# Optimization experiments

Measured on AMD Instinct MI355X. Metric: run time of the kernel, lower is better.

## Reference

```python
import jax, jax.numpy as jnp
import numpy as np

TAU = 0.07
MARGIN = 0.2
NUM_SPECIES = 64  # matches fill_max of species_ids


def _l2norm(x):
    return x / jnp.linalg.norm(x, axis=-1, keepdims=True)


def setup_inputs() -> dict:
    key = jax.random.key(0)
    k1, k2, k3 = jax.random.split(key, 3)
    B, D = 8192, 256
    species_embed = _l2norm(jax.random.normal(k1, (B, D), dtype=jnp.float32))
    text_embed = _l2norm(jax.random.normal(k2, (B, D), dtype=jnp.float32))
    species_ids = jax.random.randint(k3, (B,), 0, NUM_SPECIES, dtype=jnp.int32)
    return {"species_embed": species_embed, "text_embed": text_embed,
            "species_ids": species_ids}


def reference(species_embed, text_embed, species_ids):
    B = species_embed.shape[0]
    dtype = species_embed.dtype

    sim = species_embed @ text_embed.T                      # (B, B)
    same = species_ids[:, None] == species_ids[None, :]     # (B, B) bool, symmetric
    diag_sim = jnp.diagonal(sim)                            # (B,)

    # ---- intra-species symmetric InfoNCE (per-species CE, averaged over species)
    logits = sim / TAU
    neg_inf = jnp.finfo(dtype).min
    masked = jnp.where(same, logits, neg_inf)               # restrict to same-species cols
    diag_logit = diag_sim / TAU
    ce_v2t = jax.scipy.special.logsumexp(masked, axis=1) - diag_logit   # per-row CE
    ce_t2v = jax.scipy.special.logsumexp(masked.T, axis=1) - diag_logit # transpose: same mask is symmetric

    ones = jnp.ones((B,), dtype=dtype)
    counts = jax.ops.segment_sum(ones, species_ids, num_segments=NUM_SPECIES)          # group sizes
    seg_v2t = jax.ops.segment_sum(ce_v2t, species_ids, num_segments=NUM_SPECIES)
    seg_t2v = jax.ops.segment_sum(ce_t2v, species_ids, num_segments=NUM_SPECIES)
    valid_s = counts >= 2                                   # groups with <2 members skipped
    per_species = (seg_v2t + seg_t2v) / (2.0 * jnp.maximum(counts, 1.0))
    n_valid = jnp.maximum(jnp.sum(valid_s.astype(dtype)), 1.0)
    loss_infonce = jnp.sum(jnp.where(valid_s, per_species, 0.0)) / n_valid

    # ---- cross-species triplet (pos = mean same-species sim excl. self, neg = mean diff-species sim)
    same_f = same.astype(dtype)
    row_same_sum = jnp.sum(sim * same_f, axis=1)            # includes diagonal
    row_sum = jnp.sum(sim, axis=1)
    pos_cnt = jnp.sum(same_f, axis=1) - 1.0
    neg_cnt = B - jnp.sum(same_f, axis=1)
    pos_mean = (row_same_sum - diag_sim) / jnp.maximum(pos_cnt, 1.0)
    neg_mean = (row_sum - row_same_sum) / jnp.maximum(neg_cnt, 1.0)
    tri = jax.nn.relu(neg_mean - pos_mean + MARGIN)
    valid_i = (pos_cnt > 0) & (neg_cnt > 0)
    n_valid_i = jnp.maximum(jnp.sum(valid_i.astype(dtype)), 1.0)
    loss_triplet = jnp.sum(jnp.where(valid_i, tri, 0.0)) / n_valid_i

    return loss_infonce + loss_triplet
```

## Files before the change

### kernel.cpp

```cpp
#include <hip/hip_runtime.h>
#include <hip/hip_fp16.h>

#define TAU 0.07f
#define MARGIN 0.2f
#define NSPEC 64
#define BB 8192
#define DD 256

#define WS_SCALARS   0
#define WS_COUNTS    288
#define WS_OFFSETS   544
#define WS_LSEROW    1024
#define WS_LSECOL    33792
#define WS_TS        66560
#define WS_T         132096
#define WS_ZERO_BYTES 133120
#define WS_DIAG      133632
#define WS_MEMBER    166400
#define WS_TRI       199168

typedef _Float16 half8 __attribute__((ext_vector_type(8)));
typedef float float4v __attribute__((ext_vector_type(4)));
typedef unsigned int uint4v __attribute__((ext_vector_type(4)));

#define NB5 512
#define NB45 (NB5 + BB/4)

__device__ __forceinline__ uint4v pack8(float4 a, float4 b) {
  half8 h;
  h[0] = (_Float16)a.x; h[1] = (_Float16)a.y; h[2] = (_Float16)a.z; h[3] = (_Float16)a.w;
  h[4] = (_Float16)b.x; h[5] = (_Float16)b.y; h[6] = (_Float16)b.z; h[7] = (_Float16)b.w;
  return __builtin_bit_cast(uint4v, h);
}

__global__ void k1_all(const int* __restrict__ ids, char* ws, int* counts_g,
                       int* offsets_g, int* memberList, float* scalars) {
  __shared__ int cnt[NSPEC];
  __shared__ int off[NSPEC];
  int tid = threadIdx.x;
  float4* z = (float4*)ws;
  float4 z4 = make_float4(0.f, 0.f, 0.f, 0.f);
  for (int u = tid; u < WS_ZERO_BYTES / 16; u += 1024) z[u] = z4;
  if (tid < NSPEC) cnt[tid] = 0;
  __syncthreads();
  int myS[8], myP[8];
  #pragma unroll
  for (int r = 0; r < 8; ++r) {
    int i = r * 1024 + tid;
    int s = ids[i];
    myS[r] = s;
    myP[r] = atomicAdd(&cnt[s], 1);
  }
  __syncthreads();
  if (tid < NSPEC) {
    int o = 0;
    for (int t = 0; t < NSPEC; ++t) o += (t < tid) ? cnt[t] : 0;
    off[tid] = o;
    offsets_g[tid] = o;
    int c = cnt[tid];
    counts_g[tid] = c;
    unsigned long long bv = __ballot(c >= 2);
    float nvi = (c >= 2 && c <= BB - 1) ? (float)c : 0.f;
    for (int o2 = 1; o2 < 64; o2 <<= 1) nvi += __shfl_xor(nvi, o2);
    if (tid == 0) {
      scalars[2] = (float)__popcll(bv);
      scalars[3] = nvi;
    }
  }
  __syncthreads();
  #pragma unroll
  for (int r = 0; r < 8; ++r) {
    int i = r * 1024 + tid;
    memberList[off[myS[r]] + myP[r]] = i;
  }
}

__global__ void k2_ts(const float* __restrict__ tx, const int* __restrict__ counts,
                      const int* __restrict__ offsets, const int* __restrict__ memberList,
                      float* Ts) {
  int s = blockIdx.x, r = blockIdx.y;
  int m = counts[s], g0 = offsets[s];
  int k0 = (m * r) >> 3, k1 = (m * (r + 1)) >> 3;
  if (k0 >= k1) return;
  int d = threadIdx.x;
  float acc = 0.f;
  for (int k = k0; k < k1; ++k) acc += tx[memberList[g0 + k] * DD + d];
  atomicAdd(&Ts[s * DD + d], acc);
}

__global__ void k2b_t(const float* __restrict__ Ts, float* T) {
  int d = threadIdx.x;
  float acc = 0.f;
  for (int s = 0; s < NSPEC; ++s) acc += Ts[s * DD + d];
  T[d] = acc;
}

__global__ void k45(const float* __restrict__ sp, const float* __restrict__ tx,
                    const int* __restrict__ ids, const int* __restrict__ counts,
                    const int* __restrict__ offsets, const int* __restrict__ memberList,
                    const float* __restrict__ Ts, const float* __restrict__ T,
                    float* diag, float* tri, float* lseRow, float* lseCol) {
  __shared__ uint4v lds5[1536];
  int tid = threadIdx.x;

  if (blockIdx.x >= NB5) {
    int gt = (blockIdx.x - NB5) * 256 + tid;
    int i = gt >> 6, lane = gt & 63;
    float4 a = *reinterpret_cast<const float4*>(sp + i * DD + lane * 4);
    float4 b = *reinterpret_cast<const float4*>(tx + i * DD + lane * 4);
    float4 tv = *reinterpret_cast<const float4*>(T + lane * 4);
    int s = ids[i];
    int m = counts[s];
    float4 c = *reinterpret_cast<const float4*>(Ts + s * DD + lane * 4);
    float dDiag = a.x * b.x + a.y * b.y + a.z * b.z + a.w * b.w;
    float dT    = a.x * tv.x + a.y * tv.y + a.z * tv.z + a.w * tv.w;
    float dTs   = a.x * c.x + a.y * c.y + a.z * c.z + a.w * c.w;
    #pragma unroll
    for (int o = 1; o < 64; o <<= 1) {
      dDiag += __shfl_xor(dDiag, o);
      dT    += __shfl_xor(dT, o);
      dTs   += __shfl_xor(dTs, o);
    }
    if (lane == 0) {
      diag[i] = dDiag;
      float posMean = (dTs - dDiag) / fmaxf((float)(m - 1), 1.f);
      float negMean = (dT - dTs) / fmaxf((float)(BB - m), 1.f);
      float t = fmaxf(negMean - posMean + MARGIN, 0.f);
      tri[i] = (m >= 2 && m <= BB - 1) ? t : 0.f;
    }
    return;
  }

  int s = blockIdx.x >> 3;
  int sub = blockIdx.x & 7;
  int rt0 = sub >> 1;
  int ct0 = sub & 1;
  int m = counts[s];
  int g0 = offsets[s];
  int lane = tid & 63, wv = tid >> 6;
  int quad = lane >> 4, cl = lane & 15;

  for (int rt = rt0; rt * 64 < m; rt += 4) {
    for (int ct = ct0; ct * 128 < m; ct += 2) {
      float4v acc[8];
      #pragma unroll
      for (int cf = 0; cf < 8; ++cf) acc[cf] = (float4v){0.f, 0.f, 0.f, 0.f};

      for (int kc = 0; kc < 4; ++kc) {
        __syncthreads();
        #pragma unroll
        for (int p = 0; p < 6; ++p) {
          int u = p * 256 + tid;
          int isB = u >= 512;
          int v = isB ? (u - 512) : u;
          int row = v >> 3;
          int subu = v & 7;
          int ksl = subu >> 2, q = subu & 3;
          int d0 = kc * 64 + ksl * 32 + q * 8;
          int idx = isB ? (ct * 128 + row) : (rt * 64 + row);
          uint4v val = (uint4v){0u, 0u, 0u, 0u};
          if (idx < m) {
            const float* src = (isB ? tx : sp) + memberList[g0 + idx] * DD + d0;
            float4 f0 = *reinterpret_cast<const float4*>(src);
            float4 f1 = *reinterpret_cast<const float4*>(src + 4);
            val = pack8(f0, f1);
          }
          int qs = q ^ ((row >> 1) & 3);
          int dst = isB ? (512 + (ksl * 128 + row) * 4 + qs)
                        : ((ksl * 64 + row) * 4 + qs);
          lds5[dst] = val;
        }
        __syncthreads();
        #pragma unroll
        for (int ksl = 0; ksl < 2; ++ksl) {
          int ar = wv * 16 + cl;
          half8 a = __builtin_bit_cast(half8,
              lds5[(ksl * 64 + ar) * 4 + (quad ^ ((ar >> 1) & 3))]);
          #pragma unroll
          for (int cf = 0; cf < 8; ++cf) {
            int br = cf * 16 + cl;
            half8 b = __builtin_bit_cast(half8,
                lds5[512 + (ksl * 128 + br) * 4 + (quad ^ ((br >> 1) & 3))]);
            acc[cf] = __builtin_amdgcn_mfma_f32_16x16x32_f16(a, b, acc[cf], 0, 0, 0);
          }
        }
      }

      int riBase = rt * 64 + wv * 16 + quad * 4;
      float rowAcc[4] = {0.f, 0.f, 0.f, 0.f};
      #pragma unroll
      for (int cf = 0; cf < 8; ++cf) {
        int ci = ct * 128 + cf * 16 + cl;
        bool cv = ci < m;
        float colAcc = 0.f;
        #pragma unroll
        for (int reg = 0; reg < 4; ++reg) {
          bool rv = (riBase + reg) < m;
          float e = (rv && cv) ? __expf(acc[cf][reg] * (1.f / TAU)) : 0.f;
          rowAcc[reg] += e;
          colAcc += e;
        }
        colAcc += __shfl_xor(colAcc, 16);
        colAcc += __shfl_xor(colAcc, 32);
        if (quad == 0 && cv) atomicAdd(&lseCol[g0 + ci], colAcc);
      }
      #pragma unroll
      for (int reg = 0; reg < 4; ++reg) {
        float v = rowAcc[reg];
        v += __shfl_xor(v, 1);
        v += __shfl_xor(v, 2);
        v += __shfl_xor(v, 4);
        v += __shfl_xor(v, 8);
        if (cl == 0 && (riBase + reg) < m) atomicAdd(&lseRow[g0 + riBase + reg], v);
      }
    }
  }
}

__global__ void k67_info(const int* __restrict__ memberList, const int* __restrict__ ids,
                         const int* __restrict__ counts, const float* __restrict__ lseRow,
                         const float* __restrict__ lseCol, const float* __restrict__ diag,
                         const float* __restrict__ tri, float* scalars, float* out) {
  __shared__ float red[8];
  int g = blockIdx.x * blockDim.x + threadIdx.x;
  int i = memberList[g];
  int s = ids[i];
  int m = counts[s];
  float tt = tri[i];
  float term = 0.f;
  if (m >= 2) {
    term = (__logf(lseRow[g]) + __logf(lseCol[g]) - 2.f * diag[i] * (1.f / TAU)) /
           (2.f * (float)m);
  }
  #pragma unroll
  for (int o = 1; o < 64; o <<= 1) {
    term += __shfl_xor(term, o);
    tt += __shfl_xor(tt, o);
  }
  int wv = threadIdx.x >> 6, lane = threadIdx.x & 63;
  if (lane == 0) { red[wv] = term; red[4 + wv] = tt; }
  __syncthreads();
  if (threadIdx.x == 0) {
    atomicAdd(&scalars[1], red[0] + red[1] + red[2] + red[3]);
    atomicAdd(&scalars[0], red[4] + red[5] + red[6] + red[7]);
    __builtin_amdgcn_s_waitcnt(0);
    int old = atomicAdd((int*)&scalars[4], 1);
    if (old == (int)gridDim.x - 1) {
      float info = atomicAdd(&scalars[1], 0.f);
      float trs  = atomicAdd(&scalars[0], 0.f);
      out[0] = info / fmaxf(scalars[2], 1.f) + trs / fmaxf(scalars[3], 1.f);
    }
  }
}

extern "C" void kernel_launch(void* const* d_in, const int* in_sizes, int n_in,
                              void* d_out, int out_size, void* d_ws, size_t ws_size,
                              hipStream_t stream) {
  const float* sp = (const float*)d_in[0];
  const float* tx = (const float*)d_in[1];
  const int* ids = (const int*)d_in[2];
  float* out = (float*)d_out;

  char* ws = (char*)d_ws;
  float* scalars = (float*)(ws + WS_SCALARS);
  int* counts = (int*)(ws + WS_COUNTS);
  int* offsets = (int*)(ws + WS_OFFSETS);
  float* lseRow = (float*)(ws + WS_LSEROW);
  float* lseCol = (float*)(ws + WS_LSECOL);
  float* Ts = (float*)(ws + WS_TS);
  float* T = (float*)(ws + WS_T);
  float* diag = (float*)(ws + WS_DIAG);
  int* memberList = (int*)(ws + WS_MEMBER);
  float* tri = (float*)(ws + WS_TRI);

  k1_all<<<1, 1024, 0, stream>>>(ids, ws, counts, offsets, memberList, scalars);
  k2_ts<<<dim3(NSPEC, 8), 256, 0, stream>>>(tx, counts, offsets, memberList, Ts);
  k2b_t<<<1, 256, 0, stream>>>(Ts, T);
  k45<<<NB45, 256, 0, stream>>>(sp, tx, ids, counts, offsets, memberList, Ts, T,
                                diag, tri, lseRow, lseCol);
  k67_info<<<BB / 256, 256, 0, stream>>>(memberList, ids, counts, lseRow, lseCol,
                                         diag, tri, scalars, out);
}
```

Baseline: 111.3 us.

## Fold same-species sums into LSE tile epilogue and cut launch count

Same-species row sums of sim are now taken from the MFMA tiles already computed for the LSE, instead of a gathered per-species text-sum pass (Ts). The global text column sum T is computed by extra blocks of the first kernel and reduced by one extra block in the LSE kernel. Diagonal and triplet work moves into the final reduction kernel, and its global atomics are spread over 64 buckets. This removes two kernel launches and the gather pass, at the cost of an extra atomic per row in the tile epilogue and fp16-precision positive sums.

```diff
diff --git a/kernel.cpp b/kernel.cpp
--- a/kernel.cpp
+++ b/kernel.cpp
@@ -8,23 +8,24 @@
 #define DD 256
 
 #define WS_SCALARS   0
-#define WS_COUNTS    288
-#define WS_OFFSETS   544
-#define WS_LSEROW    1024
-#define WS_LSECOL    33792
-#define WS_TS        66560
-#define WS_T         132096
-#define WS_ZERO_BYTES 133120
-#define WS_DIAG      133632
-#define WS_MEMBER    166400
-#define WS_TRI       199168
+#define WS_BUCKET    64
+#define WS_COUNTS    8256
+#define WS_OFFSETS   8512
+#define WS_LSEROW    8768
+#define WS_LSECOL    41536
+#define WS_RAWROW    74304
+#define WS_ZERO_BYTES 107072
+#define WS_POSG      107072
+#define WS_MEMBER    139840
+#define WS_TPART     172608
+#define WS_T         303680
 
 typedef _Float16 half8 __attribute__((ext_vector_type(8)));
 typedef float float4v __attribute__((ext_vector_type(4)));
 typedef unsigned int uint4v __attribute__((ext_vector_type(4)));
 
 #define NB5 512
-#define NB45 (NB5 + BB/4)
+#define NTP 128
 
 __device__ __forceinline__ uint4v pack8(float4 a, float4 b) {
   half8 h;
@@ -33,11 +34,27 @@
   return __builtin_bit_cast(uint4v, h);
 }
 
-__global__ void k1_all(const int* __restrict__ ids, char* ws, int* counts_g,
-                       int* offsets_g, int* memberList, float* scalars) {
+__global__ void k1_all(const int* __restrict__ ids, const float* __restrict__ tx,
+                       char* ws, int* counts_g, int* offsets_g,
+                       int* memberList, int* posg, float* Tpart, float* scalars) {
+  int tid = threadIdx.x;
+  if (blockIdx.x > 0) {
+    __shared__ float part[4][256];
+    int b = blockIdx.x - 1;
+    int d = tid & 255;
+    int rq = tid >> 8;
+    int r0 = b * 64 + rq * 16;
+    float acc = 0.f;
+    #pragma unroll 4
+    for (int k = 0; k < 16; ++k) acc += tx[(r0 + k) * DD + d];
+    part[rq][d] = acc;
+    __syncthreads();
+    if (tid < 256)
+      Tpart[b * 256 + tid] = part[0][tid] + part[1][tid] + part[2][tid] + part[3][tid];
+    return;
+  }
   __shared__ int cnt[NSPEC];
   __shared__ int off[NSPEC];
-  int tid = threadIdx.x;
   float4* z = (float4*)ws;
   float4 z4 = make_float4(0.f, 0.f, 0.f, 0.f);
   for (int u = tid; u < WS_ZERO_BYTES / 16; u += 1024) z[u] = z4;
@@ -71,63 +88,24 @@
   #pragma unroll
   for (int r = 0; r < 8; ++r) {
     int i = r * 1024 + tid;
-    memberList[off[myS[r]] + myP[r]] = i;
-  }
-}
-
-__global__ void k2_ts(const float* __restrict__ tx, const int* __restrict__ counts,
-                      const int* __restrict__ offsets, const int* __restrict__ memberList,
-                      float* Ts) {
-  int s = blockIdx.x, r = blockIdx.y;
-  int m = counts[s], g0 = offsets[s];
-  int k0 = (m * r) >> 3, k1 = (m * (r + 1)) >> 3;
-  if (k0 >= k1) return;
-  int d = threadIdx.x;
-  float acc = 0.f;
-  for (int k = k0; k < k1; ++k) acc += tx[memberList[g0 + k] * DD + d];
-  atomicAdd(&Ts[s * DD + d], acc);
-}
-
-__global__ void k2b_t(const float* __restrict__ Ts, float* T) {
-  int d = threadIdx.x;
-  float acc = 0.f;
-  for (int s = 0; s < NSPEC; ++s) acc += Ts[s * DD + d];
-  T[d] = acc;
-}
-
-__global__ void k45(const float* __restrict__ sp, const float* __restrict__ tx,
-                    const int* __restrict__ ids, const int* __restrict__ counts,
-                    const int* __restrict__ offsets, const int* __restrict__ memberList,
-                    const float* __restrict__ Ts, const float* __restrict__ T,
-                    float* diag, float* tri, float* lseRow, float* lseCol) {
+    int g = off[myS[r]] + myP[r];
+    memberList[g] = i;
+    posg[i] = g;
+  }
+}
+
+__global__ void k5_lse(const float* __restrict__ sp, const float* __restrict__ tx,
+                       const int* __restrict__ counts, const int* __restrict__ offsets,
+                       const int* __restrict__ memberList,
+                       const float* __restrict__ Tpart, float* T,
+                       float* lseRow, float* lseCol, float* rawRow) {
   __shared__ uint4v lds5[1536];
   int tid = threadIdx.x;
 
-  if (blockIdx.x >= NB5) {
-    int gt = (blockIdx.x - NB5) * 256 + tid;
-    int i = gt >> 6, lane = gt & 63;
-    float4 a = *reinterpret_cast<const float4*>(sp + i * DD + lane * 4);
-    float4 b = *reinterpret_cast<const float4*>(tx + i * DD + lane * 4);
-    float4 tv = *reinterpret_cast<const float4*>(T + lane * 4);
-    int s = ids[i];
-    int m = counts[s];
-    float4 c = *reinterpret_cast<const float4*>(Ts + s * DD + lane * 4);
-    float dDiag = a.x * b.x + a.y * b.y + a.z * b.z + a.w * b.w;
-    float dT    = a.x * tv.x + a.y * tv.y + a.z * tv.z + a.w * tv.w;
-    float dTs   = a.x * c.x + a.y * c.y + a.z * c.z + a.w * c.w;
-    #pragma unroll
-    for (int o = 1; o < 64; o <<= 1) {
-      dDiag += __shfl_xor(dDiag, o);
-      dT    += __shfl_xor(dT, o);
-      dTs   += __shfl_xor(dTs, o);
-    }
-    if (lane == 0) {
-      diag[i] = dDiag;
-      float posMean = (dTs - dDiag) / fmaxf((float)(m - 1), 1.f);
-      float negMean = (dT - dTs) / fmaxf((float)(BB - m), 1.f);
-      float t = fmaxf(negMean - posMean + MARGIN, 0.f);
-      tri[i] = (m >= 2 && m <= BB - 1) ? t : 0.f;
-    }
+  if (blockIdx.x == NB5) {
+    float acc = 0.f;
+    for (int b = 0; b < NTP; ++b) acc += Tpart[b * 256 + tid];
+    T[tid] = acc;
     return;
   }
 
@@ -188,6 +166,7 @@
 
       int riBase = rt * 64 + wv * 16 + quad * 4;
       float rowAcc[4] = {0.f, 0.f, 0.f, 0.f};
+      float rawAcc[4] = {0.f, 0.f, 0.f, 0.f};
       #pragma unroll
       for (int cf = 0; cf < 8; ++cf) {
         int ci = ct * 128 + cf * 16 + cl;
@@ -196,8 +175,11 @@
         #pragma unroll
         for (int reg = 0; reg < 4; ++reg) {
           bool rv = (riBase + reg) < m;
-          float e = (rv && cv) ? __expf(acc[cf][reg] * (1.f / TAU)) : 0.f;
+          bool on = rv && cv;
+          float sv = on ? acc[cf][reg] : 0.f;
+          float e = on ? __expf(sv * (1.f / TAU)) : 0.f;
           rowAcc[reg] += e;
+          rawAcc[reg] += sv;
           colAcc += e;
         }
         colAcc += __shfl_xor(colAcc, 16);
@@ -207,49 +189,80 @@
       #pragma unroll
       for (int reg = 0; reg < 4; ++reg) {
         float v = rowAcc[reg];
-        v += __shfl_xor(v, 1);
-        v += __shfl_xor(v, 2);
-        v += __shfl_xor(v, 4);
-        v += __shfl_xor(v, 8);
-        if (cl == 0 && (riBase + reg) < m) atomicAdd(&lseRow[g0 + riBase + reg], v);
+        float w = rawAcc[reg];
+        v += __shfl_xor(v, 1);  w += __shfl_xor(w, 1);
+        v += __shfl_xor(v, 2);  w += __shfl_xor(w, 2);
+        v += __shfl_xor(v, 4);  w += __shfl_xor(w, 4);
+        v += __shfl_xor(v, 8);  w += __shfl_xor(w, 8);
+        if (cl == 0 && (riBase + reg) < m) {
+          atomicAdd(&lseRow[g0 + riBase + reg], v);
+          atomicAdd(&rawRow[g0 + riBase + reg], w);
+        }
       }
     }
   }
 }
 
-__global__ void k67_info(const int* __restrict__ memberList, const int* __restrict__ ids,
-                         const int* __restrict__ counts, const float* __restrict__ lseRow,
-                         const float* __restrict__ lseCol, const float* __restrict__ diag,
-                         const float* __restrict__ tri, float* scalars, float* out) {
+__global__ void k67_info(const float* __restrict__ sp, const float* __restrict__ tx,
+                         const int* __restrict__ ids, const int* __restrict__ counts,
+                         const int* __restrict__ posg, const float* __restrict__ T,
+                         const float* __restrict__ lseRow, const float* __restrict__ lseCol,
+                         const float* __restrict__ rawRow, char* ws, float* scalars,
+                         float* out) {
   __shared__ float red[8];
-  int g = blockIdx.x * blockDim.x + threadIdx.x;
-  int i = memberList[g];
-  int s = ids[i];
-  int m = counts[s];
-  float tt = tri[i];
-  float term = 0.f;
-  if (m >= 2) {
-    term = (__logf(lseRow[g]) + __logf(lseCol[g]) - 2.f * diag[i] * (1.f / TAU)) /
-           (2.f * (float)m);
-  }
+  __shared__ int isLast;
+  int tid = threadIdx.x;
+  int wv = tid >> 6, lane = tid & 63;
+  int i = blockIdx.x * 4 + wv;
+
+  float4 a = *reinterpret_cast<const float4*>(sp + i * DD + lane * 4);
+  float4 b = *reinterpret_cast<const float4*>(tx + i * DD + lane * 4);
+  float4 tv = *reinterpret_cast<const float4*>(T + lane * 4);
+  float dDiag = a.x * b.x + a.y * b.y + a.z * b.z + a.w * b.w;
+  float dT    = a.x * tv.x + a.y * tv.y + a.z * tv.z + a.w * tv.w;
   #pragma unroll
   for (int o = 1; o < 64; o <<= 1) {
-    term += __shfl_xor(term, o);
-    tt += __shfl_xor(tt, o);
-  }
-  int wv = threadIdx.x >> 6, lane = threadIdx.x & 63;
-  if (lane == 0) { red[wv] = term; red[4 + wv] = tt; }
-  __syncthreads();
-  if (threadIdx.x == 0) {
-    atomicAdd(&scalars[1], red[0] + red[1] + red[2] + red[3]);
-    atomicAdd(&scalars[0], red[4] + red[5] + red[6] + red[7]);
+    dDiag += __shfl_xor(dDiag, o);
+    dT    += __shfl_xor(dT, o);
+  }
+  if (lane == 0) {
+    int s = ids[i];
+    int m = counts[s];
+    int g = posg[i];
+    float rr = rawRow[g];
+    float info = 0.f;
+    if (m >= 2) {
+      info = (__logf(lseRow[g]) + __logf(lseCol[g]) - 2.f * dDiag * (1.f / TAU)) /
+             (2.f * (float)m);
+    }
+    float posMean = (rr - dDiag) / fmaxf((float)(m - 1), 1.f);
+    float negMean = (dT - rr) / fmaxf((float)(BB - m), 1.f);
+    float t = fmaxf(negMean - posMean + MARGIN, 0.f);
+    float tri = (m >= 2 && m <= BB - 1) ? t : 0.f;
+    red[wv] = info;
+    red[4 + wv] = tri;
+  }
+  __syncthreads();
+  if (tid == 0) {
+    float* bucket = (float*)(ws + WS_BUCKET + (blockIdx.x & 63) * 128);
+    atomicAdd(&bucket[0], red[0] + red[1] + red[2] + red[3]);
+    atomicAdd(&bucket[1], red[4] + red[5] + red[6] + red[7]);
     __builtin_amdgcn_s_waitcnt(0);
     int old = atomicAdd((int*)&scalars[4], 1);
-    if (old == (int)gridDim.x - 1) {
-      float info = atomicAdd(&scalars[1], 0.f);
-      float trs  = atomicAdd(&scalars[0], 0.f);
-      out[0] = info / fmaxf(scalars[2], 1.f) + trs / fmaxf(scalars[3], 1.f);
-    }
+    isLast = (old == (int)gridDim.x - 1) ? 1 : 0;
+  }
+  __syncthreads();
+  if (isLast && tid < 64) {
+    float* bucket = (float*)(ws + WS_BUCKET + tid * 128);
+    float inf = atomicAdd(&bucket[0], 0.f);
+    float trs = atomicAdd(&bucket[1], 0.f);
+    #pragma unroll
+    for (int o = 1; o < 64; o <<= 1) {
+      inf += __shfl_xor(inf, o);
+      trs += __shfl_xor(trs, o);
+    }
+    if (tid == 0)
+      out[0] = inf / fmaxf(scalars[2], 1.f) + trs / fmaxf(scalars[3], 1.f);
   }
 }
 
@@ -267,17 +280,16 @@
   int* offsets = (int*)(ws + WS_OFFSETS);
   float* lseRow = (float*)(ws + WS_LSEROW);
   float* lseCol = (float*)(ws + WS_LSECOL);
-  float* Ts = (float*)(ws + WS_TS);
+  float* rawRow = (float*)(ws + WS_RAWROW);
+  int* posg = (int*)(ws + WS_POSG);
+  int* memberList = (int*)(ws + WS_MEMBER);
+  float* Tpart = (float*)(ws + WS_TPART);
   float* T = (float*)(ws + WS_T);
-  float* diag = (float*)(ws + WS_DIAG);
-  int* memberList = (int*)(ws + WS_MEMBER);
-  float* tri = (float*)(ws + WS_TRI);
-
-  k1_all<<<1, 1024, 0, stream>>>(ids, ws, counts, offsets, memberList, scalars);
-  k2_ts<<<dim3(NSPEC, 8), 256, 0, stream>>>(tx, counts, offsets, memberList, Ts);
-  k2b_t<<<1, 256, 0, stream>>>(Ts, T);
-  k45<<<NB45, 256, 0, stream>>>(sp, tx, ids, counts, offsets, memberList, Ts, T,
-                                diag, tri, lseRow, lseCol);
-  k67_info<<<BB / 256, 256, 0, stream>>>(memberList, ids, counts, lseRow, lseCol,
-                                         diag, tri, scalars, out);
-}
+
+  k1_all<<<1 + NTP, 1024, 0, stream>>>(ids, tx, ws, counts, offsets, memberList,
+                                       posg, Tpart, scalars);
+  k5_lse<<<NB5 + 1, 256, 0, stream>>>(sp, tx, counts, offsets, memberList,
+                                      Tpart, T, lseRow, lseCol, rawRow);
+  k67_info<<<BB / 4, 256, 0, stream>>>(sp, tx, ids, counts, posg, T, lseRow, lseCol,
+                                       rawRow, ws, scalars, out);
+}
```

Result: slower. 124.9 us (+12.3%).
